# Kernel optimization log

Hardware: AMD Instinct MI355X
Metric: run time of the kernel (lower is better)

The kernel has to match this reference:

```python
import jax, jax.numpy as jnp
import numpy as np

EPS = 1e-8  # torch.nn.CosineSimilarity default eps


def setup_inputs() -> dict:
    key = jax.random.key(0)
    # [N maps, B batch, C, H, W] saliency tensors
    sal = jax.random.normal(key, (8, 32, 3, 224, 224), dtype=jnp.float32)
    return {"sal_tensor_list": sal}


def reference(sal_tensor_list):
    N, B = sal_tensor_list.shape[0], sal_tensor_list.shape[1]
    x = sal_tensor_list.reshape(N, B, -1)              # [N, B, D]
    # pairwise batched dot products: Gram over maps, per batch element
    dots = jnp.einsum('ibd,jbd->ijb', x, x)            # [N, N, B]
    norms = jnp.sqrt(jnp.sum(x * x, axis=-1))          # [N, B]
    denom = jnp.maximum(norms[:, None, :] * norms[None, :, :], EPS)
    pair_mean = jnp.abs(dots / denom).mean(axis=-1)    # [N, N] mean over batch
    # only combinations i < j (upper triangle, no diagonal)
    mask = jnp.triu(jnp.ones((N, N), dtype=bool), k=1)
    n_pairs = N * (N - 1) // 2
    return jnp.sum(jnp.where(mask, pair_mean, 0.0)) / n_pairs
```

## Files before the change

kernel.cpp:

```cpp
#include <hip/hip_runtime.h>

#define NMAPS 8
#define BATCH 32
#define DLEN  150528
#define D4    (DLEN / 4)
#define NPAIR 36
#define CHUNKS 32
#define TPB   256

__global__ __launch_bounds__(TPB) void gram_kernel(const float* __restrict__ x,
                                                   float* __restrict__ dots) {
    const int b     = blockIdx.x;
    const int chunk = blockIdx.y;
    const int tid   = threadIdx.x;

    const float4* xb = reinterpret_cast<const float4*>(x) + (size_t)b * D4;
    const size_t strideI = (size_t)BATCH * D4;

    float acc[NPAIR];
#pragma unroll
    for (int k = 0; k < NPAIR; ++k) acc[k] = 0.0f;

    for (int j = chunk * TPB + tid; j < D4; j += CHUNKS * TPB) {
        float4 v[NMAPS];
#pragma unroll
        for (int i = 0; i < NMAPS; ++i) v[i] = xb[(size_t)i * strideI + j];
        int k = 0;
#pragma unroll
        for (int i = 0; i < NMAPS; ++i) {
#pragma unroll
            for (int jj = i; jj < NMAPS; ++jj) {
                acc[k] += v[i].x * v[jj].x + v[i].y * v[jj].y +
                          v[i].z * v[jj].z + v[i].w * v[jj].w;
                ++k;
            }
        }
    }

    const int lane = tid & 63;
    const int wave = tid >> 6;
    __shared__ float red[TPB / 64][NPAIR];
#pragma unroll
    for (int k = 0; k < NPAIR; ++k) {
        float s = acc[k];
#pragma unroll
        for (int off = 32; off > 0; off >>= 1) s += __shfl_down(s, off, 64);
        if (lane == 0) red[wave][k] = s;
    }
    __syncthreads();
    if (tid < NPAIR) {
        float t = red[0][tid] + red[1][tid] + red[2][tid] + red[3][tid];
        atomicAdd(&dots[b * NPAIR + tid], t);
    }
}

__global__ __launch_bounds__(256) void finalize_kernel(const float* __restrict__ dots,
                                                       float* __restrict__ out) {
    const int tid = threadIdx.x;
    __shared__ float norms[BATCH][NMAPS];
    {
        int b = tid >> 3, i = tid & 7;
        int diag = 8 * i - (i * (i - 1)) / 2;
        norms[b][i] = sqrtf(dots[b * NPAIR + diag]);
    }
    __syncthreads();

    float sum = 0.0f;
    for (int item = tid; item < 28 * BATCH; item += 256) {
        int p = item >> 5;
        int b = item & 31;
        int i = 0, rem = p;
        while (rem >= 7 - i) { rem -= 7 - i; ++i; }
        int j = i + 1 + rem;
        int k = 8 * i - (i * (i - 1)) / 2 + (j - i);
        float d   = fabsf(dots[b * NPAIR + k]);
        float den = fmaxf(norms[b][i] * norms[b][j], 1e-8f);
        sum += d / den;
    }

    const int lane = tid & 63, wave = tid >> 6;
    __shared__ float red[4];
#pragma unroll
    for (int off = 32; off > 0; off >>= 1) sum += __shfl_down(sum, off, 64);
    if (lane == 0) red[wave] = sum;
    __syncthreads();
    if (tid == 0) {
        out[0] = (red[0] + red[1] + red[2] + red[3]) / (28.0f * BATCH);
    }
}

extern "C" void kernel_launch(void* const* d_in, const int* in_sizes, int n_in,
                              void* d_out, int out_size, void* d_ws, size_t ws_size,
                              hipStream_t stream) {
    const float* x   = (const float*)d_in[0];
    float*       out = (float*)d_out;
    float*       dots = (float*)d_ws;

    hipMemsetAsync(dots, 0, BATCH * NPAIR * sizeof(float), stream);

    dim3 grid(BATCH, CHUNKS);
    gram_kernel<<<grid, TPB, 0, stream>>>(x, dots);
    finalize_kernel<<<1, 256, 0, stream>>>(dots, out);
}
```

Measured before the change: 42.40 us.

## Software-pipeline gram loads and replace atomics/memset with per-chunk partials

The gram loop now prefetches the next strip of eight float4 loads into a second register set while computing on the current one, so more memory requests are in flight per thread. Block results go to a per-chunk partial buffer instead of atomicAdd into a zeroed buffer, which removes the memset launch. The finalize kernel sums the 32 partials per entry into shared memory. Costs are more registers, which may lower occupancy, and a larger workspace, which the code assumes is big enough.

```diff
diff --git a/kernel.cpp b/kernel.cpp
--- a/kernel.cpp
+++ b/kernel.cpp
@@ -7,9 +7,10 @@
 #define NPAIR 36
 #define CHUNKS 32
 #define TPB   256
+#define JSTRIDE (CHUNKS * TPB)
 
 __global__ __launch_bounds__(TPB) void gram_kernel(const float* __restrict__ x,
-                                                   float* __restrict__ dots) {
+                                                   float* __restrict__ partial) {
     const int b     = blockIdx.x;
     const int chunk = blockIdx.y;
     const int tid   = threadIdx.x;
@@ -21,10 +22,28 @@
 #pragma unroll
     for (int k = 0; k < NPAIR; ++k) acc[k] = 0.0f;
 
-    for (int j = chunk * TPB + tid; j < D4; j += CHUNKS * TPB) {
-        float4 v[NMAPS];
+    int j = chunk * TPB + tid;
+    float4 v[NMAPS], w[NMAPS];
 #pragma unroll
-        for (int i = 0; i < NMAPS; ++i) v[i] = xb[(size_t)i * strideI + j];
+    for (int i = 0; i < NMAPS; ++i) v[i] = xb[(size_t)i * strideI + j];
+
+    for (int j2 = j + JSTRIDE; j2 < D4; j2 += JSTRIDE) {
+#pragma unroll
+        for (int i = 0; i < NMAPS; ++i) w[i] = xb[(size_t)i * strideI + j2];
+        int k = 0;
+#pragma unroll
+        for (int i = 0; i < NMAPS; ++i) {
+#pragma unroll
+            for (int jj = i; jj < NMAPS; ++jj) {
+                acc[k] += v[i].x * v[jj].x + v[i].y * v[jj].y +
+                          v[i].z * v[jj].z + v[i].w * v[jj].w;
+                ++k;
+            }
+        }
+#pragma unroll
+        for (int i = 0; i < NMAPS; ++i) v[i] = w[i];
+    }
+    {
         int k = 0;
 #pragma unroll
         for (int i = 0; i < NMAPS; ++i) {
@@ -49,19 +68,28 @@
     }
     __syncthreads();
     if (tid < NPAIR) {
-        float t = red[0][tid] + red[1][tid] + red[2][tid] + red[3][tid];
-        atomicAdd(&dots[b * NPAIR + tid], t);
+        partial[chunk * (BATCH * NPAIR) + b * NPAIR + tid] =
+            red[0][tid] + red[1][tid] + red[2][tid] + red[3][tid];
     }
 }
 
-__global__ __launch_bounds__(256) void finalize_kernel(const float* __restrict__ dots,
+__global__ __launch_bounds__(256) void finalize_kernel(const float* __restrict__ partial,
                                                        float* __restrict__ out) {
     const int tid = threadIdx.x;
+    __shared__ float dots_s[BATCH * NPAIR];
     __shared__ float norms[BATCH][NMAPS];
+
+    for (int item = tid; item < BATCH * NPAIR; item += 256) {
+        float s = 0.0f;
+#pragma unroll
+        for (int c = 0; c < CHUNKS; ++c) s += partial[c * (BATCH * NPAIR) + item];
+        dots_s[item] = s;
+    }
+    __syncthreads();
     {
         int b = tid >> 3, i = tid & 7;
         int diag = 8 * i - (i * (i - 1)) / 2;
-        norms[b][i] = sqrtf(dots[b * NPAIR + diag]);
+        norms[b][i] = sqrtf(dots_s[b * NPAIR + diag]);
     }
     __syncthreads();
 
@@ -73,7 +101,7 @@
         while (rem >= 7 - i) { rem -= 7 - i; ++i; }
         int j = i + 1 + rem;
         int k = 8 * i - (i * (i - 1)) / 2 + (j - i);
-        float d   = fabsf(dots[b * NPAIR + k]);
+        float d   = fabsf(dots_s[b * NPAIR + k]);
         float den = fmaxf(norms[b][i] * norms[b][j], 1e-8f);
         sum += d / den;
     }
@@ -92,13 +120,11 @@
 extern "C" void kernel_launch(void* const* d_in, const int* in_sizes, int n_in,
                               void* d_out, int out_size, void* d_ws, size_t ws_size,
                               hipStream_t stream) {
-    const float* x   = (const float*)d_in[0];
-    float*       out = (float*)d_out;
-    float*       dots = (float*)d_ws;
-
-    hipMemsetAsync(dots, 0, BATCH * NPAIR * sizeof(float), stream);
+    const float* x       = (const float*)d_in[0];
+    float*       out     = (float*)d_out;
+    float*       partial = (float*)d_ws;
 
     dim3 grid(BATCH, CHUNKS);
-    gram_kernel<<<grid, TPB, 0, stream>>>(x, dots);
-    finalize_kernel<<<1, 256, 0, stream>>>(dots, out);
+    gram_kernel<<<grid, TPB, 0, stream>>>(x, partial);
+    finalize_kernel<<<1, 256, 0, stream>>>(partial, out);
 }
```

New measurement: 41.36 us. -2.4%, faster.
